# Performance work log

Hardware: AMD Instinct MI355X
Metric: run time of the kernel (lower is better)

## Reference

```python
import jax, jax.numpy as jnp
import numpy as np

DIM = 512
NUM_HEADS = 8
HEAD_SIZE = 64
INNER = NUM_HEADS * HEAD_SIZE  # 512


def setup_inputs() -> dict:
    key = jax.random.key(0)
    k1, k2, k3, k4, k5 = jax.random.split(key, 5)
    x = jax.random.normal(k1, (2, 4096, DIM), dtype=jnp.float32)
    # Linear params stored as [in, out] for y = x @ W + b (same math as torch Linear)
    w_qkv = jax.random.normal(k2, (DIM, INNER * 3), dtype=jnp.float32) * (1.0 / np.sqrt(DIM))
    b_qkv = jax.random.normal(k3, (INNER * 3,), dtype=jnp.float32) * 0.01
    w_out = jax.random.normal(k4, (INNER, DIM), dtype=jnp.float32) * (1.0 / np.sqrt(INNER))
    b_out = jax.random.normal(k5, (DIM,), dtype=jnp.float32) * 0.01
    return {"x": x, "w_qkv": w_qkv, "b_qkv": b_qkv, "w_out": w_out, "b_out": b_out}


def reference(x, w_qkv, b_qkv, w_out, b_out):
    b, n, _ = x.shape
    qkv = x @ w_qkv + b_qkv                      # [b, n, 3*inner]
    q, k, v = jnp.split(qkv, 3, axis=-1)          # each [b, n, inner]

    def heads(t):  # 'b n (h d) -> b h n d'
        return t.reshape(b, n, NUM_HEADS, HEAD_SIZE).transpose(0, 2, 1, 3)

    q, k, v = heads(q), heads(k), heads(v)
    scores = jnp.einsum('bhnd,bhmd->bhnm', q, k) / jnp.sqrt(jnp.float32(HEAD_SIZE))
    probs = jax.nn.softmax(scores, axis=-1)       # dropout is identity in eval
    out = jnp.einsum('bhnm,bhmd->bhnd', probs, v)
    out = out.transpose(0, 2, 1, 3).reshape(b, n, INNER)  # 'b h n d -> b n (h d)'
    return out @ w_out + b_out
```

## Files before the change

kernel.cpp:

```cpp
#include <hip/hip_runtime.h>

typedef __bf16 bf16;
typedef __bf16 bf16x8 __attribute__((ext_vector_type(8)));
typedef float f32x4 __attribute__((ext_vector_type(4)));
typedef unsigned u32x4 __attribute__((ext_vector_type(4)));

#define MFMA16(a, b, c) __builtin_amdgcn_mfma_f32_16x16x32_bf16((a), (b), (c), 0, 0, 0)

static __device__ __forceinline__ bf16x8 ldg8(const bf16* p) {
  return *(const bf16x8*)p;
}
static __device__ __forceinline__ unsigned cvt_pk_bf16(float lo, float hi) {
  unsigned d;
  asm("v_cvt_pk_bf16_f32 %0, %1, %2" : "=v"(d) : "v"(lo), "v"(hi));
  return d;
}
static __device__ __forceinline__ void pl32_swap(unsigned& a, unsigned& b) {
  asm("v_permlane32_swap_b32 %0, %1" : "+v"(a), "+v"(b));
}
static __device__ __forceinline__ void pl16_swap(unsigned& a, unsigned& b) {
  asm("v_permlane16_swap_b32 %0, %1" : "+v"(a), "+v"(b));
}


__global__ __launch_bounds__(256) void cvt_pack_x(const float* __restrict__ x,
                                                  bf16* __restrict__ Xp) {
  int mt = blockIdx.x, kc = blockIdx.y;
  int row = threadIdx.x >> 4;
  int c4 = (threadIdx.x & 15) * 4;
  bf16* tile = Xp + ((size_t)mt * 8 + kc) * 4096;
#pragma unroll
  for (int i = 0; i < 4; i++) {
    int r = i * 16 + row;
    const float* src = x + (size_t)(mt * 64 + r) * 512 + kc * 64 + c4;
    float4 v = *(const float4*)src;
    bf16* d = tile + r * 64 + c4;
    d[0] = (bf16)v.x; d[1] = (bf16)v.y; d[2] = (bf16)v.z; d[3] = (bf16)v.w;
  }
}

__global__ __launch_bounds__(256) void transpose_pack_w(const float* __restrict__ W,
                                                        bf16* __restrict__ Wp,
                                                        int N, int KC) {
  __shared__ bf16 tile[64][65];
  int kc = blockIdx.x, nt = blockIdx.y;
  int c = threadIdx.x & 63;
  int r4 = threadIdx.x >> 6;
#pragma unroll
  for (int i = 0; i < 16; i++) {
    int r = r4 * 16 + i;
    tile[r][c] = (bf16)W[(size_t)(kc * 64 + r) * N + nt * 64 + c];
  }
  __syncthreads();
  bf16* dst = Wp + ((size_t)nt * KC + kc) * 4096;
#pragma unroll
  for (int i = 0; i < 16; i++) {
    int r = r4 * 16 + i;
    dst[r * 64 + c] = tile[c][r];
  }
}

__device__ __forceinline__ void gemm_core_packed(const bf16* __restrict__ Ap,
                                                 const bf16* __restrict__ Bp,
                                                 int KC, bf16* Atile, bf16* Btile,
                                                 int tid, int wave, int l16,
                                                 int quad, f32x4 acc[4]) {
  for (int kc = 0; kc < KC; kc++) {
    __syncthreads();
    const bf16* ag = Ap + (size_t)kc * 4096;
    const bf16* bg = Bp + (size_t)kc * 4096;
#pragma unroll
    for (int rnd = 0; rnd < 2; rnd++) {
      int e = (rnd * 256 + tid) * 8;
      int row = e >> 6;
      int c16 = (e & 63) >> 3;
      int unit = row * 8 + (c16 ^ (row & 7));
      *(bf16x8*)&Atile[unit * 8] = ldg8(ag + e);
      *(bf16x8*)&Btile[unit * 8] = ldg8(bg + e);
    }
    __syncthreads();

    int ar = wave * 16 + l16;
    bf16x8 a0 = *(const bf16x8*)&Atile[(ar * 8 + (quad ^ (ar & 7))) * 8];
    bf16x8 a1 = *(const bf16x8*)&Atile[(ar * 8 + ((4 + quad) ^ (ar & 7))) * 8];
#pragma unroll
    for (int ct = 0; ct < 4; ct++) {
      int n = ct * 16 + l16;
      bf16x8 b0 = *(const bf16x8*)&Btile[(n * 8 + (quad ^ (n & 7))) * 8];
      bf16x8 b1 = *(const bf16x8*)&Btile[(n * 8 + ((4 + quad) ^ (n & 7))) * 8];
      acc[ct] = MFMA16(a0, b0, acc[ct]);
      acc[ct] = MFMA16(a1, b1, acc[ct]);
    }
  }
}

__global__ __launch_bounds__(256) void qkv_gemm(const bf16* __restrict__ Xp,
                                                const bf16* __restrict__ Wp1,
                                                const float* __restrict__ bqkv,
                                                bf16* __restrict__ Q,
                                                bf16* __restrict__ Kh,
                                                bf16* __restrict__ Vt) {
  int mt = blockIdx.x, nt = blockIdx.y;
  int tid = threadIdx.x;
  int wave = tid >> 6, lane = tid & 63;
  int l16 = lane & 15, quad = lane >> 4;

  __shared__ __align__(16) bf16 Atile[4096];
  __shared__ __align__(16) bf16 Btile[4096];

  f32x4 acc[4] = {};
  gemm_core_packed(Xp + (size_t)mt * 8 * 4096, Wp1 + (size_t)nt * 8 * 4096, 8,
                   Atile, Btile, tid, wave, l16, quad, acc);

#pragma unroll
  for (int ct = 0; ct < 4; ct++) {
    int c = nt * 64 + ct * 16 + l16;
    float bias = bqkv[c];
    int which = c >> 9, inner = c & 511;
    int h = inner >> 6, d = inner & 63;
#pragma unroll
    for (int r = 0; r < 4; r++) {
      int m = mt * 64 + wave * 16 + quad * 4 + r;
      int b = m >> 12, n = m & 4095;
      int bh = b * 8 + h;
      float v = acc[ct][r] + bias;
      if (which == 0)
        Q[((size_t)bh * 4096 + n) * 64 + d] = (bf16)(v * 0.18033688f);
      else if (which == 1)
        Kh[((size_t)bh * 4096 + n) * 64 + d] = (bf16)v;
      else
        Vt[(((size_t)bh * 64 + (n >> 6)) * 64 + d) * 64 + (n & 63)] = (bf16)v;
    }
  }
}

__global__ __launch_bounds__(256, 4) void flash_partial(const bf16* __restrict__ Q,
                                                        const bf16* __restrict__ K,
                                                        const bf16* __restrict__ Vt,
                                                        bf16* __restrict__ Opart,
                                                        float* __restrict__ Lpart) {
  int strip = blockIdx.x, bh = blockIdx.y, qtr = blockIdx.z;
  int tid = threadIdx.x;
  int wave = tid >> 6, lane = tid & 63;
  int l16 = lane & 15, quad = lane >> 4;

  const bf16* Qh = Q + (size_t)bh * 4096 * 64;
  const bf16* Kg = K + ((size_t)bh * 4096 + qtr * 1024) * 64;
  const bf16* Vg = Vt + (size_t)bh * 64 * 4096 + (size_t)qtr * 1024 * 64;

  __shared__ __align__(16) bf16 Klds[2][4096];
  __shared__ __align__(16) bf16 Vlds[2][4096];

  int qbase = strip * 128 + wave * 32;
  bf16x8 aq[2][2];
#pragma unroll
  for (int mt = 0; mt < 2; mt++) {
    const bf16* qr = Qh + (size_t)(qbase + mt * 16 + l16) * 64;
    aq[mt][0] = ldg8(qr + quad * 8);
    aq[mt][1] = ldg8(qr + 32 + quad * 8);
  }

  bf16x8 ones;
#pragma unroll
  for (int i = 0; i < 8; i++) ones[i] = (bf16)1.0f;

  f32x4 o[2][4] = {};
  f32x4 acc_l[2] = {};

  int e0 = tid * 8, e1 = (256 + tid) * 8;
  int r0 = e0 >> 6, r1 = e1 >> 6;
  int u0 = r0 * 8 + (((e0 & 63) >> 3) ^ (r0 & 7));
  int u1 = r1 * 8 + (((e1 & 63) >> 3) ^ (r1 & 7));

  bf16x8 kp0 = ldg8(Kg + e0), kp1 = ldg8(Kg + e1);
  bf16x8 vp0 = ldg8(Vg + e0), vp1 = ldg8(Vg + e1);

#pragma unroll 2
  for (int t = 0; t < 16; t++) {
    int cur = t & 1;
    bf16* kl = Klds[cur];
    bf16* vl = Vlds[cur];
    *(bf16x8*)&kl[u0 * 8] = kp0;
    *(bf16x8*)&kl[u1 * 8] = kp1;
    *(bf16x8*)&vl[u0 * 8] = vp0;
    *(bf16x8*)&vl[u1 * 8] = vp1;
    __syncthreads();

    if (t < 15) {
      const bf16* kg = Kg + (size_t)(t + 1) * 4096;
      const bf16* vg = Vg + (size_t)(t + 1) * 4096;
      kp0 = ldg8(kg + e0);
      kp1 = ldg8(kg + e1);
      vp0 = ldg8(vg + e0);
      vp1 = ldg8(vg + e1);
    }

#pragma unroll
    for (int h2 = 0; h2 < 2; h2++) {
      f32x4 s[2][2] = {};
      __builtin_amdgcn_s_setprio(1);
#pragma unroll
      for (int c2 = 0; c2 < 2; c2++) {
        int n = h2 * 32 + c2 * 16 + l16;
        bf16x8 k0 = *(const bf16x8*)&kl[(n * 8 + (quad ^ (n & 7))) * 8];
        bf16x8 k1 = *(const bf16x8*)&kl[(n * 8 + ((4 + quad) ^ (n & 7))) * 8];
#pragma unroll
        for (int mt = 0; mt < 2; mt++) {
          s[mt][c2] = MFMA16(k0, aq[mt][0], s[mt][c2]);
          s[mt][c2] = MFMA16(k1, aq[mt][1], s[mt][c2]);
        }
      }
      __builtin_amdgcn_s_setprio(0);

      bf16x8 pa[2];
#pragma unroll
      for (int mt = 0; mt < 2; mt++) {
        unsigned ue[2], wo[2];
#pragma unroll
        for (int c2 = 0; c2 < 2; c2++) {
          float p0 = __builtin_amdgcn_exp2f(s[mt][c2][0]);
          float p1 = __builtin_amdgcn_exp2f(s[mt][c2][1]);
          float p2 = __builtin_amdgcn_exp2f(s[mt][c2][2]);
          float p3 = __builtin_amdgcn_exp2f(s[mt][c2][3]);
          ue[c2] = cvt_pk_bf16(p0, p1);
          wo[c2] = cvt_pk_bf16(p2, p3);
        }
        pl32_swap(ue[0], ue[1]);
        pl16_swap(ue[0], ue[1]);
        pl32_swap(wo[0], wo[1]);
        pl16_swap(wo[0], wo[1]);
        u32x4 pk = {ue[0], wo[0], ue[1], wo[1]};
        pa[mt] = __builtin_bit_cast(bf16x8, pk);
      }

      __builtin_amdgcn_s_setprio(1);
      acc_l[0] = MFMA16(pa[0], ones, acc_l[0]);
      acc_l[1] = MFMA16(pa[1], ones, acc_l[1]);
#pragma unroll
      for (int ct = 0; ct < 4; ct++) {
        int d = ct * 16 + l16;
        bf16x8 bv = *(const bf16x8*)&vl[(d * 8 + ((h2 * 4 + quad) ^ (d & 7))) * 8];
        o[0][ct] = MFMA16(pa[0], bv, o[0][ct]);
        o[1][ct] = MFMA16(pa[1], bv, o[1][ct]);
      }
      __builtin_amdgcn_s_setprio(0);
    }
  }

  size_t ub = ((size_t)qtr * 16 + bh) * 32 + strip;
  bf16* op = Opart + ub * 8192;
#pragma unroll
  for (int mt = 0; mt < 2; mt++) {
#pragma unroll
    for (int ct = 0; ct < 4; ct++)
#pragma unroll
      for (int r = 0; r < 4; r++)
        op[(wave * 32 + mt * 16 + quad * 4 + r) * 64 + ct * 16 + l16] =
            (bf16)o[mt][ct][r];
    if (l16 == 0) {
#pragma unroll
      for (int r = 0; r < 4; r++)
        Lpart[ub * 128 + wave * 32 + mt * 16 + quad * 4 + r] = acc_l[mt][r];
    }
  }
}

__global__ __launch_bounds__(256) void flash_combine(const bf16* __restrict__ Opart,
                                                     const float* __restrict__ Lpart,
                                                     bf16* __restrict__ Ap) {
  int qt = blockIdx.x, bh = blockIdx.y;
  int col = threadIdx.x & 63;
  int rg = threadIdx.x >> 6;
  int strip = qt >> 1;
  int rbase = (qt & 1) * 64;
  size_t u[4];
#pragma unroll
  for (int h = 0; h < 4; h++) u[h] = ((size_t)h * 16 + bh) * 32 + strip;
  int b = bh >> 3, hh = bh & 7;
  bf16* apt = Ap + (((size_t)(b * 64 + qt)) * 8 + hh) * 4096;
#pragma unroll
  for (int i = 0; i < 16; i++) {
    int r64 = rg * 16 + i;
    int row = rbase + r64;
    float os = 0.f, ls = 0.f;
#pragma unroll
    for (int h = 0; h < 4; h++) {
      os += (float)Opart[u[h] * 8192 + row * 64 + col];
      ls += Lpart[u[h] * 128 + row];
    }
    apt[r64 * 64 + col] = (bf16)(os / ls);
  }
}

__global__ __launch_bounds__(256) void out_gemm(const bf16* __restrict__ Ap,
                                                const bf16* __restrict__ Wp2,
                                                const float* __restrict__ bout,
                                                float* __restrict__ Out) {
  int mt = blockIdx.x, nt = blockIdx.y;
  int tid = threadIdx.x;
  int wave = tid >> 6, lane = tid & 63;
  int l16 = lane & 15, quad = lane >> 4;

  __shared__ __align__(16) bf16 Atile[4096];
  __shared__ __align__(16) bf16 Btile[4096];

  f32x4 acc[4] = {};
  gemm_core_packed(Ap + (size_t)mt * 8 * 4096, Wp2 + (size_t)nt * 8 * 4096, 8,
                   Atile, Btile, tid, wave, l16, quad, acc);

#pragma unroll
  for (int ct = 0; ct < 4; ct++) {
    int c = nt * 64 + ct * 16 + l16;
    float bias = bout[c];
#pragma unroll
    for (int r = 0; r < 4; r++) {
      int m = mt * 64 + wave * 16 + quad * 4 + r;
      Out[(size_t)m * 512 + c] = acc[ct][r] + bias;
    }
  }
}

extern "C" void kernel_launch(void* const* d_in, const int* in_sizes, int n_in,
                              void* d_out, int out_size, void* d_ws,
                              size_t ws_size, hipStream_t stream) {
  const float* x = (const float*)d_in[0];
  const float* w_qkv = (const float*)d_in[1];
  const float* b_qkv = (const float*)d_in[2];
  const float* w_out = (const float*)d_in[3];
  const float* b_out = (const float*)d_in[4];
  float* out = (float*)d_out;

  char* ws = (char*)d_ws;
  bf16* Q = (bf16*)(ws + 0);
  bf16* K = (bf16*)(ws + 8388608);
  bf16* Vt = (bf16*)(ws + 16777216);
  bf16* Wp2 = (bf16*)(ws + 25165824);
  bf16* Opart = (bf16*)(ws + 25690112);
  float* Lpart = (float*)(ws + 59244544);
  bf16* Xp = (bf16*)(ws + 25690112);
  bf16* Wp1 = (bf16*)(ws + 34078720);
  bf16* Ap = (bf16*)(ws + 0);

  cvt_pack_x<<<dim3(128, 8), 256, 0, stream>>>(x, Xp);
  transpose_pack_w<<<dim3(8, 24), 256, 0, stream>>>(w_qkv, Wp1, 1536, 8);
  transpose_pack_w<<<dim3(8, 8), 256, 0, stream>>>(w_out, Wp2, 512, 8);
  qkv_gemm<<<dim3(128, 24), 256, 0, stream>>>(Xp, Wp1, b_qkv, Q, K, Vt);
  flash_partial<<<dim3(32, 16, 4), 256, 0, stream>>>(Q, K, Vt, Opart, Lpart);
  flash_combine<<<dim3(64, 16), 256, 0, stream>>>(Opart, Lpart, Ap);
  out_gemm<<<dim3(128, 8), 256, 0, stream>>>(Ap, Wp2, b_out, out);
}
```

Measured before the change: 204.5 us.

## Use 128x128 double-buffered GEMMs, 2-way KV split, and vectorized packing

The QKV and output GEMMs move from 64x64 tiles with a 64-wide K chunk to 128x128 tiles with a 32-wide K chunk, double-buffered in LDS with register prefetch. This raises per-wave MFMA reuse and cuts global traffic. The flash kernel splits keys two ways instead of four, and its inner loop is restructured so both halves' scores are computed before the softmax and PV MFMAs. The pack and combine kernels write vectorized 8-wide bf16 stores in a new K-major layout. Risks are fewer blocks for occupancy, more register pressure from the larger accumulators, and the unswizzled LDS layout, which may cause bank conflicts.

```diff
diff --git a/kernel.cpp b/kernel.cpp
--- a/kernel.cpp
+++ b/kernel.cpp
@@ -26,110 +26,136 @@
 __global__ __launch_bounds__(256) void cvt_pack_x(const float* __restrict__ x,
                                                   bf16* __restrict__ Xp) {
   int mt = blockIdx.x, kc = blockIdx.y;
-  int row = threadIdx.x >> 4;
-  int c4 = (threadIdx.x & 15) * 4;
-  bf16* tile = Xp + ((size_t)mt * 8 + kc) * 4096;
-#pragma unroll
-  for (int i = 0; i < 4; i++) {
-    int r = i * 16 + row;
-    const float* src = x + (size_t)(mt * 64 + r) * 512 + kc * 64 + c4;
-    float4 v = *(const float4*)src;
-    bf16* d = tile + r * 64 + c4;
-    d[0] = (bf16)v.x; d[1] = (bf16)v.y; d[2] = (bf16)v.z; d[3] = (bf16)v.w;
-  }
+  int r = threadIdx.x >> 1;
+  int khalf = threadIdx.x & 1;
+  const float* src = x + (size_t)(mt * 128 + r) * 512 + kc * 32 + khalf * 16;
+  float4 v0 = *(const float4*)(src + 0);
+  float4 v1 = *(const float4*)(src + 4);
+  float4 v2 = *(const float4*)(src + 8);
+  float4 v3 = *(const float4*)(src + 12);
+  bf16* tile = Xp + ((size_t)mt * 16 + kc) * 4096;
+  bf16x8 a, b;
+  a[0] = (bf16)v0.x; a[1] = (bf16)v0.y; a[2] = (bf16)v0.z; a[3] = (bf16)v0.w;
+  a[4] = (bf16)v1.x; a[5] = (bf16)v1.y; a[6] = (bf16)v1.z; a[7] = (bf16)v1.w;
+  b[0] = (bf16)v2.x; b[1] = (bf16)v2.y; b[2] = (bf16)v2.z; b[3] = (bf16)v2.w;
+  b[4] = (bf16)v3.x; b[5] = (bf16)v3.y; b[6] = (bf16)v3.z; b[7] = (bf16)v3.w;
+  int kc0 = khalf * 2;
+  *(bf16x8*)&tile[(kc0 + 0) * 1024 + r * 8] = a;
+  *(bf16x8*)&tile[(kc0 + 1) * 1024 + r * 8] = b;
 }
 
 __global__ __launch_bounds__(256) void transpose_pack_w(const float* __restrict__ W,
                                                         bf16* __restrict__ Wp,
-                                                        int N, int KC) {
-  __shared__ bf16 tile[64][65];
+                                                        int N) {
+  __shared__ float tile[32 * 129];
   int kc = blockIdx.x, nt = blockIdx.y;
-  int c = threadIdx.x & 63;
-  int r4 = threadIdx.x >> 6;
-#pragma unroll
-  for (int i = 0; i < 16; i++) {
-    int r = r4 * 16 + i;
-    tile[r][c] = (bf16)W[(size_t)(kc * 64 + r) * N + nt * 64 + c];
+  int row = threadIdx.x >> 3;
+  int c0 = (threadIdx.x & 7) * 16;
+  const float* src = W + (size_t)(kc * 32 + row) * N + nt * 128 + c0;
+#pragma unroll
+  for (int i = 0; i < 4; i++) {
+    float4 v = *(const float4*)(src + i * 4);
+    tile[row * 129 + c0 + i * 4 + 0] = v.x;
+    tile[row * 129 + c0 + i * 4 + 1] = v.y;
+    tile[row * 129 + c0 + i * 4 + 2] = v.z;
+    tile[row * 129 + c0 + i * 4 + 3] = v.w;
   }
   __syncthreads();
-  bf16* dst = Wp + ((size_t)nt * KC + kc) * 4096;
-#pragma unroll
-  for (int i = 0; i < 16; i++) {
-    int r = r4 * 16 + i;
-    dst[r * 64 + c] = tile[c][r];
-  }
-}
-
-__device__ __forceinline__ void gemm_core_packed(const bf16* __restrict__ Ap,
-                                                 const bf16* __restrict__ Bp,
-                                                 int KC, bf16* Atile, bf16* Btile,
-                                                 int tid, int wave, int l16,
-                                                 int quad, f32x4 acc[4]) {
-  for (int kc = 0; kc < KC; kc++) {
+  bf16* dst = Wp + ((size_t)nt * 16 + kc) * 4096;
+#pragma unroll
+  for (int half = 0; half < 2; half++) {
+    int U = threadIdx.x + half * 256;
+    int kchunk = U >> 7, n = U & 127;
+    bf16x8 o;
+#pragma unroll
+    for (int j = 0; j < 8; j++) o[j] = (bf16)tile[(kchunk * 8 + j) * 129 + n];
+    *(bf16x8*)&dst[U * 8] = o;
+  }
+}
+
+__device__ __forceinline__ void gemm128_core(const bf16* __restrict__ At,
+                                             const bf16* __restrict__ Bt,
+                                             bf16* Ab0, bf16* Ab1, bf16* Bb0,
+                                             bf16* Bb1, int tid, int wr, int wc,
+                                             int l16, int quad, f32x4 acc[4][4]) {
+  bf16x8 pa0 = ldg8(At + tid * 8);
+  bf16x8 pa1 = ldg8(At + 2048 + tid * 8);
+  bf16x8 pb0 = ldg8(Bt + tid * 8);
+  bf16x8 pb1 = ldg8(Bt + 2048 + tid * 8);
+#pragma unroll 2
+  for (int kc = 0; kc < 16; kc++) {
+    bf16* Ab = (kc & 1) ? Ab1 : Ab0;
+    bf16* Bb = (kc & 1) ? Bb1 : Bb0;
+    *(bf16x8*)&Ab[tid * 8] = pa0;
+    *(bf16x8*)&Ab[2048 + tid * 8] = pa1;
+    *(bf16x8*)&Bb[tid * 8] = pb0;
+    *(bf16x8*)&Bb[2048 + tid * 8] = pb1;
     __syncthreads();
-    const bf16* ag = Ap + (size_t)kc * 4096;
-    const bf16* bg = Bp + (size_t)kc * 4096;
-#pragma unroll
-    for (int rnd = 0; rnd < 2; rnd++) {
-      int e = (rnd * 256 + tid) * 8;
-      int row = e >> 6;
-      int c16 = (e & 63) >> 3;
-      int unit = row * 8 + (c16 ^ (row & 7));
-      *(bf16x8*)&Atile[unit * 8] = ldg8(ag + e);
-      *(bf16x8*)&Btile[unit * 8] = ldg8(bg + e);
-    }
-    __syncthreads();
-
-    int ar = wave * 16 + l16;
-    bf16x8 a0 = *(const bf16x8*)&Atile[(ar * 8 + (quad ^ (ar & 7))) * 8];
-    bf16x8 a1 = *(const bf16x8*)&Atile[(ar * 8 + ((4 + quad) ^ (ar & 7))) * 8];
-#pragma unroll
-    for (int ct = 0; ct < 4; ct++) {
-      int n = ct * 16 + l16;
-      bf16x8 b0 = *(const bf16x8*)&Btile[(n * 8 + (quad ^ (n & 7))) * 8];
-      bf16x8 b1 = *(const bf16x8*)&Btile[(n * 8 + ((4 + quad) ^ (n & 7))) * 8];
-      acc[ct] = MFMA16(a0, b0, acc[ct]);
-      acc[ct] = MFMA16(a1, b1, acc[ct]);
-    }
-  }
-}
-
-__global__ __launch_bounds__(256) void qkv_gemm(const bf16* __restrict__ Xp,
-                                                const bf16* __restrict__ Wp1,
-                                                const float* __restrict__ bqkv,
-                                                bf16* __restrict__ Q,
-                                                bf16* __restrict__ Kh,
-                                                bf16* __restrict__ Vt) {
+    if (kc < 15) {
+      const bf16* an = At + (kc + 1) * 4096;
+      const bf16* bn = Bt + (kc + 1) * 4096;
+      pa0 = ldg8(an + tid * 8);
+      pa1 = ldg8(an + 2048 + tid * 8);
+      pb0 = ldg8(bn + tid * 8);
+      pb1 = ldg8(bn + 2048 + tid * 8);
+    }
+    bf16x8 af[4], bf[4];
+#pragma unroll
+    for (int fi = 0; fi < 4; fi++)
+      af[fi] = *(const bf16x8*)&Ab[(quad * 128 + wr * 64 + fi * 16 + l16) * 8];
+#pragma unroll
+    for (int fj = 0; fj < 4; fj++)
+      bf[fj] = *(const bf16x8*)&Bb[(quad * 128 + wc * 64 + fj * 16 + l16) * 8];
+    __builtin_amdgcn_s_setprio(1);
+#pragma unroll
+    for (int fi = 0; fi < 4; fi++)
+#pragma unroll
+      for (int fj = 0; fj < 4; fj++)
+        acc[fi][fj] = MFMA16(af[fi], bf[fj], acc[fi][fj]);
+    __builtin_amdgcn_s_setprio(0);
+  }
+}
+
+__global__ __launch_bounds__(256, 3) void qkv_gemm(const bf16* __restrict__ Xp,
+                                                   const bf16* __restrict__ Wp1,
+                                                   const float* __restrict__ bqkv,
+                                                   bf16* __restrict__ Q,
+                                                   bf16* __restrict__ Kh,
+                                                   bf16* __restrict__ Vt) {
   int mt = blockIdx.x, nt = blockIdx.y;
   int tid = threadIdx.x;
   int wave = tid >> 6, lane = tid & 63;
   int l16 = lane & 15, quad = lane >> 4;
-
-  __shared__ __align__(16) bf16 Atile[4096];
-  __shared__ __align__(16) bf16 Btile[4096];
-
-  f32x4 acc[4] = {};
-  gemm_core_packed(Xp + (size_t)mt * 8 * 4096, Wp1 + (size_t)nt * 8 * 4096, 8,
-                   Atile, Btile, tid, wave, l16, quad, acc);
-
-#pragma unroll
-  for (int ct = 0; ct < 4; ct++) {
-    int c = nt * 64 + ct * 16 + l16;
+  int wr = wave >> 1, wc = wave & 1;
+
+  __shared__ __align__(16) bf16 Ab[2][4096];
+  __shared__ __align__(16) bf16 Bb[2][4096];
+
+  f32x4 acc[4][4] = {};
+  gemm128_core(Xp + (size_t)mt * 16 * 4096, Wp1 + (size_t)nt * 16 * 4096,
+               Ab[0], Ab[1], Bb[0], Bb[1], tid, wr, wc, l16, quad, acc);
+
+#pragma unroll
+  for (int fj = 0; fj < 4; fj++) {
+    int c = nt * 128 + wc * 64 + fj * 16 + l16;
     float bias = bqkv[c];
     int which = c >> 9, inner = c & 511;
     int h = inner >> 6, d = inner & 63;
 #pragma unroll
-    for (int r = 0; r < 4; r++) {
-      int m = mt * 64 + wave * 16 + quad * 4 + r;
-      int b = m >> 12, n = m & 4095;
-      int bh = b * 8 + h;
-      float v = acc[ct][r] + bias;
-      if (which == 0)
-        Q[((size_t)bh * 4096 + n) * 64 + d] = (bf16)(v * 0.18033688f);
-      else if (which == 1)
-        Kh[((size_t)bh * 4096 + n) * 64 + d] = (bf16)v;
-      else
-        Vt[(((size_t)bh * 64 + (n >> 6)) * 64 + d) * 64 + (n & 63)] = (bf16)v;
+    for (int fi = 0; fi < 4; fi++) {
+#pragma unroll
+      for (int r = 0; r < 4; r++) {
+        int m = mt * 128 + wr * 64 + fi * 16 + quad * 4 + r;
+        int b = m >> 12, n = m & 4095;
+        int bh = b * 8 + h;
+        float v = acc[fi][fj][r] + bias;
+        if (which == 0)
+          Q[((size_t)bh * 4096 + n) * 64 + d] = (bf16)(v * 0.18033688f);
+        else if (which == 1)
+          Kh[((size_t)bh * 4096 + n) * 64 + d] = (bf16)v;
+        else
+          Vt[(((size_t)bh * 64 + (n >> 6)) * 64 + d) * 64 + (n & 63)] = (bf16)v;
+      }
     }
   }
 }
@@ -139,14 +165,14 @@
                                                         const bf16* __restrict__ Vt,
                                                         bf16* __restrict__ Opart,
                                                         float* __restrict__ Lpart) {
-  int strip = blockIdx.x, bh = blockIdx.y, qtr = blockIdx.z;
+  int strip = blockIdx.x, bh = blockIdx.y, half = blockIdx.z;
   int tid = threadIdx.x;
   int wave = tid >> 6, lane = tid & 63;
   int l16 = lane & 15, quad = lane >> 4;
 
   const bf16* Qh = Q + (size_t)bh * 4096 * 64;
-  const bf16* Kg = K + ((size_t)bh * 4096 + qtr * 1024) * 64;
-  const bf16* Vg = Vt + (size_t)bh * 64 * 4096 + (size_t)qtr * 1024 * 64;
+  const bf16* Kg = K + ((size_t)bh * 4096 + half * 2048) * 64;
+  const bf16* Vg = Vt + (size_t)bh * 64 * 4096 + (size_t)half * 2048 * 64;
 
   __shared__ __align__(16) bf16 Klds[2][4096];
   __shared__ __align__(16) bf16 Vlds[2][4096];
@@ -176,7 +202,7 @@
   bf16x8 vp0 = ldg8(Vg + e0), vp1 = ldg8(Vg + e1);
 
 #pragma unroll 2
-  for (int t = 0; t < 16; t++) {
+  for (int t = 0; t < 32; t++) {
     int cur = t & 1;
     bf16* kl = Klds[cur];
     bf16* vl = Vlds[cur];
@@ -186,7 +212,7 @@
     *(bf16x8*)&vl[u1 * 8] = vp1;
     __syncthreads();
 
-    if (t < 15) {
+    if (t < 31) {
       const bf16* kg = Kg + (size_t)(t + 1) * 4096;
       const bf16* vg = Vg + (size_t)(t + 1) * 4096;
       kp0 = ldg8(kg + e0);
@@ -195,10 +221,10 @@
       vp1 = ldg8(vg + e1);
     }
 
-#pragma unroll
-    for (int h2 = 0; h2 < 2; h2++) {
-      f32x4 s[2][2] = {};
-      __builtin_amdgcn_s_setprio(1);
+    f32x4 s[2][2][2] = {};
+    __builtin_amdgcn_s_setprio(1);
+#pragma unroll
+    for (int h2 = 0; h2 < 2; h2++)
 #pragma unroll
       for (int c2 = 0; c2 < 2; c2++) {
         int n = h2 * 32 + c2 * 16 + l16;
@@ -206,22 +232,24 @@
         bf16x8 k1 = *(const bf16x8*)&kl[(n * 8 + ((4 + quad) ^ (n & 7))) * 8];
 #pragma unroll
         for (int mt = 0; mt < 2; mt++) {
-          s[mt][c2] = MFMA16(k0, aq[mt][0], s[mt][c2]);
-          s[mt][c2] = MFMA16(k1, aq[mt][1], s[mt][c2]);
+          s[h2][mt][c2] = MFMA16(k0, aq[mt][0], s[h2][mt][c2]);
+          s[h2][mt][c2] = MFMA16(k1, aq[mt][1], s[h2][mt][c2]);
         }
       }
-      __builtin_amdgcn_s_setprio(0);
-
-      bf16x8 pa[2];
+    __builtin_amdgcn_s_setprio(0);
+
+    bf16x8 pa[2][2];
+#pragma unroll
+    for (int h2 = 0; h2 < 2; h2++)
 #pragma unroll
       for (int mt = 0; mt < 2; mt++) {
         unsigned ue[2], wo[2];
 #pragma unroll
         for (int c2 = 0; c2 < 2; c2++) {
-          float p0 = __builtin_amdgcn_exp2f(s[mt][c2][0]);
-          float p1 = __builtin_amdgcn_exp2f(s[mt][c2][1]);
-          float p2 = __builtin_amdgcn_exp2f(s[mt][c2][2]);
-          float p3 = __builtin_amdgcn_exp2f(s[mt][c2][3]);
+          float p0 = __builtin_amdgcn_exp2f(s[h2][mt][c2][0]);
+          float p1 = __builtin_amdgcn_exp2f(s[h2][mt][c2][1]);
+          float p2 = __builtin_amdgcn_exp2f(s[h2][mt][c2][2]);
+          float p3 = __builtin_amdgcn_exp2f(s[h2][mt][c2][3]);
           ue[c2] = cvt_pk_bf16(p0, p1);
           wo[c2] = cvt_pk_bf16(p2, p3);
         }
@@ -230,24 +258,27 @@
         pl32_swap(wo[0], wo[1]);
         pl16_swap(wo[0], wo[1]);
         u32x4 pk = {ue[0], wo[0], ue[1], wo[1]};
-        pa[mt] = __builtin_bit_cast(bf16x8, pk);
-      }
-
-      __builtin_amdgcn_s_setprio(1);
-      acc_l[0] = MFMA16(pa[0], ones, acc_l[0]);
-      acc_l[1] = MFMA16(pa[1], ones, acc_l[1]);
+        pa[h2][mt] = __builtin_bit_cast(bf16x8, pk);
+      }
+
+    __builtin_amdgcn_s_setprio(1);
+    acc_l[0] = MFMA16(pa[0][0], ones, acc_l[0]);
+    acc_l[1] = MFMA16(pa[0][1], ones, acc_l[1]);
+    acc_l[0] = MFMA16(pa[1][0], ones, acc_l[0]);
+    acc_l[1] = MFMA16(pa[1][1], ones, acc_l[1]);
+#pragma unroll
+    for (int h2 = 0; h2 < 2; h2++)
 #pragma unroll
       for (int ct = 0; ct < 4; ct++) {
         int d = ct * 16 + l16;
         bf16x8 bv = *(const bf16x8*)&vl[(d * 8 + ((h2 * 4 + quad) ^ (d & 7))) * 8];
-        o[0][ct] = MFMA16(pa[0], bv, o[0][ct]);
-        o[1][ct] = MFMA16(pa[1], bv, o[1][ct]);
-      }
-      __builtin_amdgcn_s_setprio(0);
-    }
-  }
-
-  size_t ub = ((size_t)qtr * 16 + bh) * 32 + strip;
+        o[0][ct] = MFMA16(pa[h2][0], bv, o[0][ct]);
+        o[1][ct] = MFMA16(pa[h2][1], bv, o[1][ct]);
+      }
+    __builtin_amdgcn_s_setprio(0);
+  }
+
+  size_t ub = ((size_t)half * 16 + bh) * 32 + strip;
   bf16* op = Opart + ub * 8192;
 #pragma unroll
   for (int mt = 0; mt < 2; mt++) {
@@ -268,54 +299,56 @@
 __global__ __launch_bounds__(256) void flash_combine(const bf16* __restrict__ Opart,
                                                      const float* __restrict__ Lpart,
                                                      bf16* __restrict__ Ap) {
-  int qt = blockIdx.x, bh = blockIdx.y;
-  int col = threadIdx.x & 63;
-  int rg = threadIdx.x >> 6;
-  int strip = qt >> 1;
-  int rbase = (qt & 1) * 64;
-  size_t u[4];
-#pragma unroll
-  for (int h = 0; h < 4; h++) u[h] = ((size_t)h * 16 + bh) * 32 + strip;
-  int b = bh >> 3, hh = bh & 7;
-  bf16* apt = Ap + (((size_t)(b * 64 + qt)) * 8 + hh) * 4096;
-#pragma unroll
-  for (int i = 0; i < 16; i++) {
-    int r64 = rg * 16 + i;
-    int row = rbase + r64;
-    float os = 0.f, ls = 0.f;
-#pragma unroll
-    for (int h = 0; h < 4; h++) {
-      os += (float)Opart[u[h] * 8192 + row * 64 + col];
-      ls += Lpart[u[h] * 128 + row];
-    }
-    apt[r64 * 64 + col] = (bf16)(os / ls);
-  }
-}
-
-__global__ __launch_bounds__(256) void out_gemm(const bf16* __restrict__ Ap,
-                                                const bf16* __restrict__ Wp2,
-                                                const float* __restrict__ bout,
-                                                float* __restrict__ Out) {
+  int mt = blockIdx.x, kc = blockIdx.y;
+  int b = mt >> 5, strip = mt & 31;
+  int h = kc >> 1, d0 = (kc & 1) * 32;
+  int bh = b * 8 + h;
+  size_t u0 = (size_t)bh * 32 + strip;
+  size_t u1 = ((size_t)16 + bh) * 32 + strip;
+  bf16* dst = Ap + ((size_t)mt * 16 + kc) * 4096;
+#pragma unroll
+  for (int hf = 0; hf < 2; hf++) {
+    int U = threadIdx.x + hf * 256;
+    int kchunk = U >> 7, r = U & 127;
+    bf16x8 o0 = ldg8(&Opart[u0 * 8192 + r * 64 + d0 + kchunk * 8]);
+    bf16x8 o1 = ldg8(&Opart[u1 * 8192 + r * 64 + d0 + kchunk * 8]);
+    float ls = Lpart[u0 * 128 + r] + Lpart[u1 * 128 + r];
+    float rl = 1.0f / ls;
+    bf16x8 ov;
+#pragma unroll
+    for (int j = 0; j < 8; j++) ov[j] = (bf16)(((float)o0[j] + (float)o1[j]) * rl);
+    *(bf16x8*)&dst[U * 8] = ov;
+  }
+}
+
+__global__ __launch_bounds__(256, 3) void out_gemm(const bf16* __restrict__ Ap,
+                                                   const bf16* __restrict__ Wp2,
+                                                   const float* __restrict__ bout,
+                                                   float* __restrict__ Out) {
   int mt = blockIdx.x, nt = blockIdx.y;
   int tid = threadIdx.x;
   int wave = tid >> 6, lane = tid & 63;
   int l16 = lane & 15, quad = lane >> 4;
-
-  __shared__ __align__(16) bf16 Atile[4096];
-  __shared__ __align__(16) bf16 Btile[4096];
-
-  f32x4 acc[4] = {};
-  gemm_core_packed(Ap + (size_t)mt * 8 * 4096, Wp2 + (size_t)nt * 8 * 4096, 8,
-                   Atile, Btile, tid, wave, l16, quad, acc);
-
-#pragma unroll
-  for (int ct = 0; ct < 4; ct++) {
-    int c = nt * 64 + ct * 16 + l16;
+  int wr = wave >> 1, wc = wave & 1;
+
+  __shared__ __align__(16) bf16 Ab[2][4096];
+  __shared__ __align__(16) bf16 Bb[2][4096];
+
+  f32x4 acc[4][4] = {};
+  gemm128_core(Ap + (size_t)mt * 16 * 4096, Wp2 + (size_t)nt * 16 * 4096,
+               Ab[0], Ab[1], Bb[0], Bb[1], tid, wr, wc, l16, quad, acc);
+
+#pragma unroll
+  for (int fj = 0; fj < 4; fj++) {
+    int c = nt * 128 + wc * 64 + fj * 16 + l16;
     float bias = bout[c];
 #pragma unroll
-    for (int r = 0; r < 4; r++) {
-      int m = mt * 64 + wave * 16 + quad * 4 + r;
-      Out[(size_t)m * 512 + c] = acc[ct][r] + bias;
+    for (int fi = 0; fi < 4; fi++) {
+#pragma unroll
+      for (int r = 0; r < 4; r++) {
+        int m = mt * 128 + wr * 64 + fi * 16 + quad * 4 + r;
+        Out[(size_t)m * 512 + c] = acc[fi][fj][r] + bias;
+      }
     }
   }
 }
@@ -336,16 +369,16 @@
   bf16* Vt = (bf16*)(ws + 16777216);
   bf16* Wp2 = (bf16*)(ws + 25165824);
   bf16* Opart = (bf16*)(ws + 25690112);
-  float* Lpart = (float*)(ws + 59244544);
-  bf16* Xp = (bf16*)(ws + 25690112);
-  bf16* Wp1 = (bf16*)(ws + 34078720);
-  bf16* Ap = (bf16*)(ws + 0);
-
-  cvt_pack_x<<<dim3(128, 8), 256, 0, stream>>>(x, Xp);
-  transpose_pack_w<<<dim3(8, 24), 256, 0, stream>>>(w_qkv, Wp1, 1536, 8);
-  transpose_pack_w<<<dim3(8, 8), 256, 0, stream>>>(w_out, Wp2, 512, 8);
-  qkv_gemm<<<dim3(128, 24), 256, 0, stream>>>(Xp, Wp1, b_qkv, Q, K, Vt);
-  flash_partial<<<dim3(32, 16, 4), 256, 0, stream>>>(Q, K, Vt, Opart, Lpart);
+  float* Lpart = (float*)(ws + 42467328);
+  bf16* Xp = (bf16*)(ws + 42991616);
+  bf16* Wp1 = (bf16*)(ws + 51380224);
+  bf16* Ap = (bf16*)(ws + 52953088);
+
+  cvt_pack_x<<<dim3(64, 16), 256, 0, stream>>>(x, Xp);
+  transpose_pack_w<<<dim3(16, 12), 256, 0, stream>>>(w_qkv, Wp1, 1536);
+  transpose_pack_w<<<dim3(16, 4), 256, 0, stream>>>(w_out, Wp2, 512);
+  qkv_gemm<<<dim3(64, 12), 256, 0, stream>>>(Xp, Wp1, b_qkv, Q, K, Vt);
+  flash_partial<<<dim3(32, 16, 2), 256, 0, stream>>>(Q, K, Vt, Opart, Lpart);
   flash_combine<<<dim3(64, 16), 256, 0, stream>>>(Opart, Lpart, Ap);
-  out_gemm<<<dim3(128, 8), 256, 0, stream>>>(Ap, Wp2, b_out, out);
-}
+  out_gemm<<<dim3(64, 4), 256, 0, stream>>>(Ap, Wp2, b_out, out);
+}
```

New measurement: 206.5 us. Within noise of the previous version (+1.0%).
